# Kernel tuning notes

Hardware: AMD Instinct MI355X
Metric: run time of the kernel (lower is better)

## Reference

```python
import jax, jax.numpy as jnp
import numpy as np

B, N, D_IN, D_MID, D_OUT = 512, 8192, 128, 256, 16


def setup_inputs() -> dict:
    key = jax.random.key(0)
    k1, k2, k3, k4, k5 = jax.random.split(key, 5)
    return {
        "x": jax.random.normal(k1, (B, D_IN), dtype=jnp.float32),
        "calc_X": jax.random.normal(k2, (N, D_IN), dtype=jnp.float32),
        "calc_Y": jax.random.normal(k3, (N, D_OUT), dtype=jnp.float32),
        "W1": jax.random.normal(k4, (D_MID, D_IN), dtype=jnp.float32) * (D_IN ** -0.5),
        "W2": jax.random.normal(k5, (D_OUT, D_MID), dtype=jnp.float32) * (D_MID ** -0.5),
        "h": jnp.array([1.5], dtype=jnp.float32),
    }


def _mlp(v, W1, W2):
    # fc2(relu(fc1(v))), both linears bias-free
    return jnp.maximum(v @ W1.T, 0.0) @ W2.T


def reference(x, calc_X, calc_Y, W1, W2, h):
    Zw = _mlp(x, W1, W2)        # [B, D_OUT] queries
    Xw = _mlp(calc_X, W1, W2)   # [N, D_OUT] reference embeddings (batched, no loop)
    # Gaussian kernel weights gauss((Xw_j - Zw)/h): [B, N, D_OUT]
    z = (Xw[None, :, :] - Zw[:, None, :]) / h
    w = jnp.exp(-0.5 * z * z)
    denominator = jnp.sum(w, axis=1)                   # [B, D_OUT]
    numerator = jnp.einsum("bnd,nd->bd", w, calc_Y)    # [B, D_OUT]
    return numerator / denominator
```

## Files before the change

### kernel.cpp

```cpp
#include <hip/hip_runtime.h>

#define D_IN  128
#define D_MID 256
#define D_OUT 16
#define NB    512
#define NN    8192
#define NROWS (NB + NN)
#define RPB   16
#define BT    8
#define NSLICE 8
#define SLICE_N (NN / NSLICE)

#define EW_OFF    0
#define PART_OFF  (NROWS * D_OUT)
#define W1T_OFF   (PART_OFF + 2 * NSLICE * NB * D_OUT)
#define W2T_OFF   (W1T_OFF + D_MID * D_IN)

__global__ __launch_bounds__(256) void transpose_kernel(
    const float* __restrict__ W1, const float* __restrict__ W2,
    float* __restrict__ W1T, float* __restrict__ W2T)
{
    const int tid = blockIdx.x * 256 + threadIdx.x;
    if (tid < 8192) {
        const int k4 = tid >> 8;
        const int j  = tid & 255;
        const float4 v = reinterpret_cast<const float4*>(W1)[(size_t)j * 32 + k4];
        reinterpret_cast<float4*>(W1T)[(size_t)k4 * 256 + j] = v;
    } else {
        const int t2 = tid - 8192;
        const int j4 = t2 >> 4;
        const int d  = t2 & 15;
        const float4 v = reinterpret_cast<const float4*>(W2)[(size_t)d * 64 + j4];
        reinterpret_cast<float4*>(W2T)[(size_t)j4 * 16 + d] = v;
    }
}

__global__ __launch_bounds__(256) void mlp_kernel(
    const float* __restrict__ x, const float* __restrict__ calc_X,
    const float* __restrict__ W1T, const float* __restrict__ W2T,
    const float* __restrict__ hptr, float* __restrict__ Ews)
{
    __shared__ float hid[RPB][260];

    const int t = threadIdx.x;
    const int row0 = blockIdx.x * RPB;

    const float* __restrict__ rbase = (row0 < NB)
        ? (x + (size_t)row0 * D_IN)
        : (calc_X + (size_t)(row0 - NB) * D_IN);
    const float4* __restrict__ row4 = reinterpret_cast<const float4*>(rbase);
    const float4* __restrict__ w1t4 = reinterpret_cast<const float4*>(W1T);

    float acc[RPB] = {};
#pragma unroll 2
    for (int k4 = 0; k4 < 32; ++k4) {
        const float4 wv = w1t4[k4 * 256 + t];
#pragma unroll
        for (int r = 0; r < RPB; ++r) {
            const float4 rv = row4[r * 32 + k4];
            acc[r] = fmaf(rv.x, wv.x, fmaf(rv.y, wv.y,
                     fmaf(rv.z, wv.z, fmaf(rv.w, wv.w, acc[r]))));
        }
    }
#pragma unroll
    for (int r = 0; r < RPB; ++r)
        hid[r][t] = fmaxf(acc[r], 0.f);
    __syncthreads();

    {
        const int r = t >> 4;
        const int d = t & 15;
        const float4* __restrict__ w2t4 = reinterpret_cast<const float4*>(W2T);
        float4 a = make_float4(0.f, 0.f, 0.f, 0.f);
#pragma unroll 8
        for (int j4 = 0; j4 < 64; ++j4) {
            const float4 wv = w2t4[j4 * 16 + d];
            const float4 hv = *reinterpret_cast<const float4*>(&hid[r][j4 * 4]);
            a.x = fmaf(hv.x, wv.x, a.x);
            a.y = fmaf(hv.y, wv.y, a.y);
            a.z = fmaf(hv.z, wv.z, a.z);
            a.w = fmaf(hv.w, wv.w, a.w);
        }
        const float s = 0.84932180028801904272f / hptr[0];
        Ews[(size_t)(row0 + r) * D_OUT + d] = ((a.x + a.y) + (a.z + a.w)) * s;
    }
}

__global__ __launch_bounds__(256) void kde_kernel(
    const float* __restrict__ Ews, const float* __restrict__ Y,
    float* __restrict__ partial)
{
    __shared__ float red[4][16][16];

    const int t     = threadIdx.x;
    const int d     = t & 15;
    const int chunk = t >> 4;
    const int b0    = blockIdx.x * BT;
    const int slice = blockIdx.y;
    const float* __restrict__ Xws = Ews + (size_t)NB * D_OUT;

    float z[BT], num[BT] = {}, den[BT] = {};
#pragma unroll
    for (int bt = 0; bt < BT; ++bt)
        z[bt] = Ews[(size_t)(b0 + bt) * D_OUT + d];

#pragma unroll 4
    for (int i = 0; i < SLICE_N / 16; ++i) {
        const int n = slice * SLICE_N + i * 16 + chunk;
        const float xw = Xws[(size_t)n * D_OUT + d];
        const float yv = Y[(size_t)n * D_OUT + d];
#pragma unroll
        for (int bt = 0; bt < BT; ++bt) {
            const float df = xw - z[bt];
            const float w  = __builtin_amdgcn_exp2f(-(df * df));
            den[bt] += w;
            num[bt] = fmaf(w, yv, num[bt]);
        }
    }

    float vals[16];
#pragma unroll
    for (int bt = 0; bt < BT; ++bt) {
        vals[bt * 2 + 0] = num[bt];
        vals[bt * 2 + 1] = den[bt];
    }
#pragma unroll
    for (int m = 16; m <= 32; m <<= 1) {
#pragma unroll
        for (int v = 0; v < 16; ++v)
            vals[v] += __shfl_xor(vals[v], m, 64);
    }

    const int wave = t >> 6;
    if ((t & 63) < 16) {
#pragma unroll
        for (int v = 0; v < 16; ++v) red[wave][d][v] = vals[v];
    }
    __syncthreads();

    {
        const int p  = t & 1;
        const int dd = (t >> 1) & 15;
        const int bt = t >> 5;
        const int v  = bt * 2 + p;
        const float sum = red[0][dd][v] + red[1][dd][v] + red[2][dd][v] + red[3][dd][v];
        partial[(size_t)(p * NSLICE + slice) * NB * D_OUT + (size_t)(b0 + bt) * D_OUT + dd] = sum;
    }
}

__global__ __launch_bounds__(256) void combine_kernel(
    const float* __restrict__ partial, float* __restrict__ out)
{
    const int i = blockIdx.x * 256 + threadIdx.x;
    float nsum = 0.f, dsum = 0.f;
#pragma unroll
    for (int s = 0; s < NSLICE; ++s) {
        nsum += partial[(size_t)s * NB * D_OUT + i];
        dsum += partial[(size_t)(NSLICE + s) * NB * D_OUT + i];
    }
    out[i] = nsum / dsum;
}

extern "C" void kernel_launch(void* const* d_in, const int* in_sizes, int n_in,
                              void* d_out, int out_size, void* d_ws, size_t ws_size,
                              hipStream_t stream) {
    const float* x      = (const float*)d_in[0];
    const float* calc_X = (const float*)d_in[1];
    const float* calc_Y = (const float*)d_in[2];
    const float* W1     = (const float*)d_in[3];
    const float* W2     = (const float*)d_in[4];
    const float* h      = (const float*)d_in[5];

    float* ws      = (float*)d_ws;
    float* Ews     = ws + EW_OFF;
    float* partial = ws + PART_OFF;
    float* W1T     = ws + W1T_OFF;
    float* W2T     = ws + W2T_OFF;
    float* out     = (float*)d_out;

    transpose_kernel<<<dim3(36), dim3(256), 0, stream>>>(W1, W2, W1T, W2T);
    mlp_kernel<<<dim3(NROWS / RPB), dim3(256), 0, stream>>>(x, calc_X, W1T, W2T, h, Ews);
    kde_kernel<<<dim3(NB / BT, NSLICE), dim3(256), 0, stream>>>(Ews, calc_Y, partial);
    combine_kernel<<<dim3(NB * D_OUT / 256), dim3(256), 0, stream>>>(partial, out);
}
```

Measured before the change: 54.71 us.

## Move fc1 to split-bf16 MFMA, expand KDE exponent algebraically, retile KDE

```diff
diff --git a/kernel.cpp b/kernel.cpp
--- a/kernel.cpp
+++ b/kernel.cpp
@@ -6,28 +6,68 @@
 #define NB    512
 #define NN    8192
 #define NROWS (NB + NN)
-#define RPB   16
-#define BT    8
-#define NSLICE 8
+#define BT    16
+#define NSLICE 16
 #define SLICE_N (NN / NSLICE)
 
-#define EW_OFF    0
-#define PART_OFF  (NROWS * D_OUT)
-#define W1T_OFF   (PART_OFF + 2 * NSLICE * NB * D_OUT)
-#define W2T_OFF   (W1T_OFF + D_MID * D_IN)
-
-__global__ __launch_bounds__(256) void transpose_kernel(
+typedef __attribute__((ext_vector_type(8))) short bf16x8;
+typedef __attribute__((ext_vector_type(8))) unsigned short u16x8;
+typedef __attribute__((ext_vector_type(4))) float f32x4;
+
+#define HID_OFF   0
+#define ZQ_OFF    2228224
+#define TARR_OFF  2236416
+#define ANEG_OFF  2367488
+#define PART_OFF  2498560
+#define W2T_OFF   2760704
+#define BF16_OFF  2764800
+#define W1HI_OFF  0
+#define W1LO_OFF  32768
+#define XHI_OFF   65536
+#define XLO_OFF   1179648
+
+__device__ inline void cvt_hilo(float f, unsigned short& hi, unsigned short& lo) {
+    unsigned u = __builtin_bit_cast(unsigned, f);
+    unsigned r = (u + 0x7FFFu + ((u >> 16) & 1u)) >> 16;
+    hi = (unsigned short)r;
+    const float fh = __builtin_bit_cast(float, r << 16);
+    const float fl = f - fh;
+    unsigned ul = __builtin_bit_cast(unsigned, fl);
+    unsigned rl = (ul + 0x7FFFu + ((ul >> 16) & 1u)) >> 16;
+    lo = (unsigned short)rl;
+}
+
+__global__ __launch_bounds__(256) void prep_kernel(
+    const float* __restrict__ x, const float* __restrict__ calc_X,
     const float* __restrict__ W1, const float* __restrict__ W2,
-    float* __restrict__ W1T, float* __restrict__ W2T)
+    unsigned short* __restrict__ W1hi, unsigned short* __restrict__ W1lo,
+    unsigned short* __restrict__ Xhi, unsigned short* __restrict__ Xlo,
+    float* __restrict__ W2T)
 {
     const int tid = blockIdx.x * 256 + threadIdx.x;
-    if (tid < 8192) {
-        const int k4 = tid >> 8;
-        const int j  = tid & 255;
-        const float4 v = reinterpret_cast<const float4*>(W1)[(size_t)j * 32 + k4];
-        reinterpret_cast<float4*>(W1T)[(size_t)k4 * 256 + j] = v;
+    if (tid < 4096) {
+        const size_t e = (size_t)tid * 8;
+        const float4 a = reinterpret_cast<const float4*>(W1 + e)[0];
+        const float4 b = reinterpret_cast<const float4*>(W1 + e)[1];
+        const float f[8] = {a.x, a.y, a.z, a.w, b.x, b.y, b.z, b.w};
+        u16x8 hv, lv;
+#pragma unroll
+        for (int i = 0; i < 8; ++i) { unsigned short h, l; cvt_hilo(f[i], h, l); hv[i] = h; lv[i] = l; }
+        *reinterpret_cast<u16x8*>(W1hi + e) = hv;
+        *reinterpret_cast<u16x8*>(W1lo + e) = lv;
+    } else if (tid < 143360) {
+        const size_t e = (size_t)(tid - 4096) * 8;
+        const float* src = (e < (size_t)NB * D_IN) ? (x + e) : (calc_X + e - (size_t)NB * D_IN);
+        const float4 a = reinterpret_cast<const float4*>(src)[0];
+        const float4 b = reinterpret_cast<const float4*>(src)[1];
+        const float f[8] = {a.x, a.y, a.z, a.w, b.x, b.y, b.z, b.w};
+        u16x8 hv, lv;
+#pragma unroll
+        for (int i = 0; i < 8; ++i) { unsigned short h, l; cvt_hilo(f[i], h, l); hv[i] = h; lv[i] = l; }
+        *reinterpret_cast<u16x8*>(Xhi + e) = hv;
+        *reinterpret_cast<u16x8*>(Xlo + e) = lv;
     } else {
-        const int t2 = tid - 8192;
+        const int t2 = tid - 143360;
         const int j4 = t2 >> 4;
         const int d  = t2 & 15;
         const float4 v = reinterpret_cast<const float4*>(W2)[(size_t)d * 64 + j4];
@@ -35,90 +75,176 @@
     }
 }
 
-__global__ __launch_bounds__(256) void mlp_kernel(
+__global__ __launch_bounds__(256) void fc1_kernel(
+    const unsigned short* __restrict__ Xhi, const unsigned short* __restrict__ Xlo,
+    const unsigned short* __restrict__ W1hi, const unsigned short* __restrict__ W1lo,
+    float* __restrict__ hidden)
+{
+    const int t    = threadIdx.x;
+    const int wv   = t >> 6;
+    const int lane = t & 63;
+    const int rb   = blockIdx.x >> 2;
+    const int ch   = blockIdx.x & 3;
+    const int l15  = lane & 15;
+    const int kb   = lane >> 4;
+
+    const int m = rb * 64 + wv * 16 + l15;
+    bf16x8 ahi[4], alo[4];
+#pragma unroll
+    for (int ks = 0; ks < 4; ++ks) {
+        const size_t off = (size_t)m * D_IN + ks * 32 + kb * 8;
+        ahi[ks] = *reinterpret_cast<const bf16x8*>(Xhi + off);
+        alo[ks] = *reinterpret_cast<const bf16x8*>(Xlo + off);
+    }
+
+    f32x4 acc[4];
+#pragma unroll
+    for (int nt = 0; nt < 4; ++nt) acc[nt] = f32x4{0.f, 0.f, 0.f, 0.f};
+
+#pragma unroll
+    for (int ks = 0; ks < 4; ++ks) {
+        bf16x8 bhi[4], blo[4];
+#pragma unroll
+        for (int nt = 0; nt < 4; ++nt) {
+            const int n = ch * 64 + nt * 16 + l15;
+            const size_t off = (size_t)n * D_IN + ks * 32 + kb * 8;
+            bhi[nt] = *reinterpret_cast<const bf16x8*>(W1hi + off);
+            blo[nt] = *reinterpret_cast<const bf16x8*>(W1lo + off);
+        }
+#pragma unroll
+        for (int nt = 0; nt < 4; ++nt) {
+            acc[nt] = __builtin_amdgcn_mfma_f32_16x16x32_bf16(ahi[ks], bhi[nt], acc[nt], 0, 0, 0);
+            acc[nt] = __builtin_amdgcn_mfma_f32_16x16x32_bf16(alo[ks], bhi[nt], acc[nt], 0, 0, 0);
+            acc[nt] = __builtin_amdgcn_mfma_f32_16x16x32_bf16(ahi[ks], blo[nt], acc[nt], 0, 0, 0);
+        }
+    }
+
+    const int mrow = rb * 64 + wv * 16 + kb * 4;
+#pragma unroll
+    for (int nt = 0; nt < 4; ++nt) {
+        const int n = ch * 64 + nt * 16 + l15;
+#pragma unroll
+        for (int r = 0; r < 4; ++r)
+            hidden[(size_t)(mrow + r) * D_MID + n] = fmaxf(acc[nt][r], 0.f);
+    }
+}
+
+__global__ __launch_bounds__(256) void fcheck_kernel(
     const float* __restrict__ x, const float* __restrict__ calc_X,
-    const float* __restrict__ W1T, const float* __restrict__ W2T,
-    const float* __restrict__ hptr, float* __restrict__ Ews)
-{
-    __shared__ float hid[RPB][260];
-
-    const int t = threadIdx.x;
-    const int row0 = blockIdx.x * RPB;
-
-    const float* __restrict__ rbase = (row0 < NB)
-        ? (x + (size_t)row0 * D_IN)
-        : (calc_X + (size_t)(row0 - NB) * D_IN);
-    const float4* __restrict__ row4 = reinterpret_cast<const float4*>(rbase);
-    const float4* __restrict__ w1t4 = reinterpret_cast<const float4*>(W1T);
-
-    float acc[RPB] = {};
-#pragma unroll 2
-    for (int k4 = 0; k4 < 32; ++k4) {
-        const float4 wv = w1t4[k4 * 256 + t];
-#pragma unroll
-        for (int r = 0; r < RPB; ++r) {
-            const float4 rv = row4[r * 32 + k4];
-            acc[r] = fmaf(rv.x, wv.x, fmaf(rv.y, wv.y,
-                     fmaf(rv.z, wv.z, fmaf(rv.w, wv.w, acc[r]))));
+    const float* __restrict__ W1, float* __restrict__ hidden)
+{
+    __shared__ int sflag;
+    const int t    = threadIdx.x;
+    const int rb   = blockIdx.x >> 2;
+    const int ch   = blockIdx.x & 3;
+    const int row0 = rb * 64;
+    if (t == 0) sflag = 0;
+    __syncthreads();
+
+    if (t < 64) {
+        const int r = row0 + 5;
+        const int j = ch * 64 + t;
+        const float* __restrict__ rowp = (r < NB) ? (x + (size_t)r * D_IN)
+                                                  : (calc_X + (size_t)(r - NB) * D_IN);
+        const float* __restrict__ w1r = W1 + (size_t)j * D_IN;
+        float a = 0.f;
+#pragma unroll 4
+        for (int k = 0; k < D_IN; ++k) a = fmaf(rowp[k], w1r[k], a);
+        a = fmaxf(a, 0.f);
+        const float got = hidden[(size_t)r * D_MID + j];
+        if (fabsf(a - got) > 1e-2f * fmaxf(1.f, fabsf(a))) sflag = 1;
+    }
+    __syncthreads();
+    if (!sflag) return;
+
+    const int j = ch * 64 + (t & 63);
+    const float* __restrict__ w1r = W1 + (size_t)j * D_IN;
+    for (int rr = (t >> 6) * 16; rr < (t >> 6) * 16 + 16; ++rr) {
+        const int r = row0 + rr;
+        const float* __restrict__ rowp = (r < NB) ? (x + (size_t)r * D_IN)
+                                                  : (calc_X + (size_t)(r - NB) * D_IN);
+        float a = 0.f;
+#pragma unroll 4
+        for (int k = 0; k < D_IN; ++k) a = fmaf(rowp[k], w1r[k], a);
+        hidden[(size_t)r * D_MID + j] = fmaxf(a, 0.f);
+    }
+}
+
+__global__ __launch_bounds__(256) void fc2_kernel(
+    const float* __restrict__ hidden, const float* __restrict__ W2T,
+    const float* __restrict__ hptr,
+    float* __restrict__ zq, float* __restrict__ tarr, float* __restrict__ aneg)
+{
+    const int t    = threadIdx.x;
+    const int rloc = t >> 5;
+    const int half = (t >> 4) & 1;
+    const int d    = t & 15;
+    const int r    = blockIdx.x * 8 + rloc;
+
+    const float4* __restrict__ h4 =
+        reinterpret_cast<const float4*>(hidden + (size_t)r * D_MID) + half * 32;
+    const float4* __restrict__ w4 =
+        reinterpret_cast<const float4*>(W2T) + half * 32 * 16;
+
+    float4 a = make_float4(0.f, 0.f, 0.f, 0.f);
+#pragma unroll 8
+    for (int j4 = 0; j4 < 32; ++j4) {
+        const float4 hv = h4[j4];
+        const float4 wv = w4[j4 * 16 + d];
+        a.x = fmaf(hv.x, wv.x, a.x);
+        a.y = fmaf(hv.y, wv.y, a.y);
+        a.z = fmaf(hv.z, wv.z, a.z);
+        a.w = fmaf(hv.w, wv.w, a.w);
+    }
+    float v = (a.x + a.y) + (a.z + a.w);
+    v += __shfl_xor(v, 16, 64);
+    if (half == 0) {
+        const float s = 0.84932180028801904272f / hptr[0];
+        const float z = v * s;
+        if (r < NB) {
+            zq[(size_t)r * D_OUT + d] = z;
+        } else {
+            const size_t k = (size_t)(r - NB) * D_OUT + d;
+            tarr[k] = z + z;
+            aneg[k] = -z * z;
         }
     }
-#pragma unroll
-    for (int r = 0; r < RPB; ++r)
-        hid[r][t] = fmaxf(acc[r], 0.f);
-    __syncthreads();
-
-    {
-        const int r = t >> 4;
-        const int d = t & 15;
-        const float4* __restrict__ w2t4 = reinterpret_cast<const float4*>(W2T);
-        float4 a = make_float4(0.f, 0.f, 0.f, 0.f);
-#pragma unroll 8
-        for (int j4 = 0; j4 < 64; ++j4) {
-            const float4 wv = w2t4[j4 * 16 + d];
-            const float4 hv = *reinterpret_cast<const float4*>(&hid[r][j4 * 4]);
-            a.x = fmaf(hv.x, wv.x, a.x);
-            a.y = fmaf(hv.y, wv.y, a.y);
-            a.z = fmaf(hv.z, wv.z, a.z);
-            a.w = fmaf(hv.w, wv.w, a.w);
-        }
-        const float s = 0.84932180028801904272f / hptr[0];
-        Ews[(size_t)(row0 + r) * D_OUT + d] = ((a.x + a.y) + (a.z + a.w)) * s;
-    }
 }
 
 __global__ __launch_bounds__(256) void kde_kernel(
-    const float* __restrict__ Ews, const float* __restrict__ Y,
+    const float* __restrict__ zq, const float* __restrict__ tarr,
+    const float* __restrict__ aneg, const float* __restrict__ Y,
     float* __restrict__ partial)
 {
-    __shared__ float red[4][16][16];
+    __shared__ float red[4][16][32];
 
     const int t     = threadIdx.x;
     const int d     = t & 15;
     const int chunk = t >> 4;
     const int b0    = blockIdx.x * BT;
     const int slice = blockIdx.y;
-    const float* __restrict__ Xws = Ews + (size_t)NB * D_OUT;
 
     float z[BT], num[BT] = {}, den[BT] = {};
 #pragma unroll
     for (int bt = 0; bt < BT; ++bt)
-        z[bt] = Ews[(size_t)(b0 + bt) * D_OUT + d];
-
-#pragma unroll 4
+        z[bt] = zq[(size_t)(b0 + bt) * D_OUT + d];
+
+#pragma unroll 2
     for (int i = 0; i < SLICE_N / 16; ++i) {
-        const int n = slice * SLICE_N + i * 16 + chunk;
-        const float xw = Xws[(size_t)n * D_OUT + d];
-        const float yv = Y[(size_t)n * D_OUT + d];
+        const size_t n = (size_t)slice * SLICE_N + i * 16 + chunk;
+        const float tv = tarr[n * D_OUT + d];
+        const float av = aneg[n * D_OUT + d];
+        const float yv = Y[n * D_OUT + d];
 #pragma unroll
         for (int bt = 0; bt < BT; ++bt) {
-            const float df = xw - z[bt];
-            const float w  = __builtin_amdgcn_exp2f(-(df * df));
-            den[bt] += w;
-            num[bt] = fmaf(w, yv, num[bt]);
+            const float e = fmaf(tv, z[bt], av);
+            const float u = __builtin_amdgcn_exp2f(e);
+            den[bt] += u;
+            num[bt] = fmaf(u, yv, num[bt]);
         }
     }
 
-    float vals[16];
+    float vals[32];
 #pragma unroll
     for (int bt = 0; bt < BT; ++bt) {
         vals[bt * 2 + 0] = num[bt];
@@ -127,21 +253,23 @@
 #pragma unroll
     for (int m = 16; m <= 32; m <<= 1) {
 #pragma unroll
-        for (int v = 0; v < 16; ++v)
+        for (int v = 0; v < 32; ++v)
             vals[v] += __shfl_xor(vals[v], m, 64);
     }
 
     const int wave = t >> 6;
     if ((t & 63) < 16) {
 #pragma unroll
-        for (int v = 0; v < 16; ++v) red[wave][d][v] = vals[v];
+        for (int v = 0; v < 32; ++v) red[wave][d][v] = vals[v];
     }
     __syncthreads();
 
-    {
-        const int p  = t & 1;
-        const int dd = (t >> 1) & 15;
-        const int bt = t >> 5;
+#pragma unroll
+    for (int rep = 0; rep < 2; ++rep) {
+        const int o  = rep * 256 + t;
+        const int p  = o & 1;
+        const int dd = (o >> 1) & 15;
+        const int bt = o >> 5;
         const int v  = bt * 2 + p;
         const float sum = red[0][dd][v] + red[1][dd][v] + red[2][dd][v] + red[3][dd][v];
         partial[(size_t)(p * NSLICE + slice) * NB * D_OUT + (size_t)(b0 + bt) * D_OUT + dd] = sum;
@@ -172,14 +300,24 @@
     const float* h      = (const float*)d_in[5];
 
     float* ws      = (float*)d_ws;
-    float* Ews     = ws + EW_OFF;
+    float* hidden  = ws + HID_OFF;
+    float* zq      = ws + ZQ_OFF;
+    float* tarr    = ws + TARR_OFF;
+    float* aneg    = ws + ANEG_OFF;
     float* partial = ws + PART_OFF;
-    float* W1T     = ws + W1T_OFF;
     float* W2T     = ws + W2T_OFF;
-    float* out     = (float*)d_out;
-
-    transpose_kernel<<<dim3(36), dim3(256), 0, stream>>>(W1, W2, W1T, W2T);
-    mlp_kernel<<<dim3(NROWS / RPB), dim3(256), 0, stream>>>(x, calc_X, W1T, W2T, h, Ews);
-    kde_kernel<<<dim3(NB / BT, NSLICE), dim3(256), 0, stream>>>(Ews, calc_Y, partial);
+    unsigned short* bf = (unsigned short*)(ws + BF16_OFF);
+    unsigned short* W1hi = bf + W1HI_OFF;
+    unsigned short* W1lo = bf + W1LO_OFF;
+    unsigned short* Xhi  = bf + XHI_OFF;
+    unsigned short* Xlo  = bf + XLO_OFF;
+    float* out = (float*)d_out;
+
+    prep_kernel<<<dim3(564), dim3(256), 0, stream>>>(x, calc_X, W1, W2,
+                                                     W1hi, W1lo, Xhi, Xlo, W2T);
+    fc1_kernel<<<dim3(544), dim3(256), 0, stream>>>(Xhi, Xlo, W1hi, W1lo, hidden);
+    fcheck_kernel<<<dim3(544), dim3(256), 0, stream>>>(x, calc_X, W1, hidden);
+    fc2_kernel<<<dim3(NROWS / 8), dim3(256), 0, stream>>>(hidden, W2T, h, zq, tarr, aneg);
+    kde_kernel<<<dim3(NB / BT, NSLICE), dim3(256), 0, stream>>>(zq, tarr, aneg, calc_Y, partial);
     combine_kernel<<<dim3(NB * D_OUT / 256), dim3(256), 0, stream>>>(partial, out);
 }
```

After: 60.18 us. 1.1x slower.
